# Kernel optimization log

Measured on AMD Instinct MI355X. Metric: run time of the kernel, lower is better.

## Reference

```python
import jax, jax.numpy as jnp
import numpy as np

NUM_USERS = 100000
NUM_ITEMS = 200000
IN_DIM = 128
HID = 256
E = 500000


def setup_inputs() -> dict:
    key = jax.random.key(0)
    ks = jax.random.split(key, 12)
    s1 = 1.0 / np.sqrt(2 * IN_DIM)
    s2 = 1.0 / np.sqrt(HID)
    return {
        "user_embed": jax.random.normal(ks[0], (NUM_USERS, IN_DIM), jnp.float32),
        "item_embed": jax.random.normal(ks[1], (NUM_ITEMS, IN_DIM), jnp.float32),
        "u_clicks": jax.random.randint(ks[2], (E,), 0, NUM_USERS, jnp.int32),
        "v_clicks": jax.random.randint(ks[3], (E,), 0, NUM_ITEMS, jnp.int32),
        "u_buys": jax.random.randint(ks[4], (E,), 0, NUM_USERS, jnp.int32),
        "v_buys": jax.random.randint(ks[5], (E,), 0, NUM_ITEMS, jnp.int32),
        "W1_clicks": jax.random.normal(ks[6], (2 * IN_DIM, HID), jnp.float32) * s1,
        "b1_clicks": jnp.zeros((HID,), jnp.float32),
        "W2_clicks": jax.random.normal(ks[7], (HID,), jnp.float32) * s2,
        "b2_clicks": jnp.zeros((1,), jnp.float32),
        "W1_buys": jax.random.normal(ks[8], (2 * IN_DIM, HID), jnp.float32) * s1,
        "b1_buys": jnp.zeros((HID,), jnp.float32),
        "W2_buys": jax.random.normal(ks[9], (HID,), jnp.float32) * s2,
        "b2_buys": jnp.zeros((1,), jnp.float32),
    }


def _edge_mlp(h_u, h_v, W1, b1, W2, b2):
    # concat([h_u, h_v]) @ W1 computed without materializing the concat:
    # split W1 into source-half and target-half. Dropout(p=0) is identity.
    d = h_u.shape[1]
    h = jax.nn.relu(h_u @ W1[:d] + h_v @ W1[d:] + b1)  # [E, HID]
    return h @ W2 + b2[0]  # [E] (Linear(hidden,1).squeeze(1))


def reference(user_embed, item_embed, u_clicks, v_clicks, u_buys, v_buys,
              W1_clicks, b1_clicks, W2_clicks, b2_clicks,
              W1_buys, b1_buys, W2_buys, b2_buys):
    logits_clicks = _edge_mlp(user_embed[u_clicks], item_embed[v_clicks],
                              W1_clicks, b1_clicks, W2_clicks, b2_clicks)
    logits_buys = _edge_mlp(user_embed[u_buys], item_embed[v_buys],
                            W1_buys, b1_buys, W2_buys, b2_buys)
    return logits_clicks, logits_buys
```

## Files before the change

### kernel.cpp

```cpp
#include <hip/hip_runtime.h>
#include <hip/hip_bf16.h>

typedef short bf16x8 __attribute__((ext_vector_type(8)));
typedef float f32x4 __attribute__((ext_vector_type(4)));

#define HID 256
#define IN_DIM 128
#define M_BLOCK 64

__device__ __forceinline__ float bf2f(unsigned short x) {
    union { unsigned int u; float f; } c; c.u = ((unsigned int)x) << 16; return c.f;
}
__device__ __forceinline__ unsigned short f2bf(float f) {
    union { float f; unsigned int u; } c; c.f = f;
    unsigned int u = c.u;
    u += 0x7FFFu + ((u >> 16) & 1u);
    return (unsigned short)(u >> 16);
}
__device__ __forceinline__ unsigned int pack2(float lo, float hi) {
    return (unsigned int)f2bf(lo) | ((unsigned int)f2bf(hi) << 16);
}

__device__ __forceinline__ void gload_lds16(const void* g, void* l) {
    __builtin_amdgcn_global_load_lds(
        (const __attribute__((address_space(1))) void*)g,
        (__attribute__((address_space(3))) void*)l,
        16, 0, 0);
}

__device__ __forceinline__ bool detect_bf16(const unsigned short* p, int strideElems) {
    const int lane = threadIdx.x & 63;
    unsigned int u = p[(size_t)2 * lane * strideElems];
    unsigned int e = (u >> 7) & 0xFFu;
    bool bad = ((u & 0x7FFFu) != 0u) && (e < 90u || e > 141u);
    return __ballot(bad) == 0ull;
}
__device__ __forceinline__ bool detect_idx64(const int* p) {
    const int lane = threadIdx.x & 63;
    int v = p[2 * (lane * 64) + 1];
    return __ballot(v != 0) == 0ull;
}

extern "C" __global__ void cvt_tables_kernel(
    const void* __restrict__ user_embed, const void* __restrict__ item_embed,
    unsigned short* __restrict__ uT, unsigned short* __restrict__ iT,
    long long nU8, long long nI8)
{
    const int t = blockIdx.y;
    const void* src = t ? item_embed : user_embed;
    unsigned short* dst = t ? iT : uT;
    const long long n8 = t ? nI8 : nU8;
    const bool bf = detect_bf16((const unsigned short*)src, 1024);
    long long i = (long long)blockIdx.x * 256 + threadIdx.x;
    const long long stride = (long long)gridDim.x * 256;
    if (bf) {
        const uint4* s = (const uint4*)src;
        for (; i < n8; i += stride)
            *reinterpret_cast<uint4*>(dst + i * 8) = s[i];
    } else {
        const float4* s = (const float4*)src;
        for (; i < n8; i += stride) {
            float4 f0 = s[2 * i];
            float4 f1 = s[2 * i + 1];
            uint4 o;
            o.x = pack2(f0.x, f0.y);
            o.y = pack2(f0.z, f0.w);
            o.z = pack2(f1.x, f1.y);
            o.w = pack2(f1.z, f1.w);
            *reinterpret_cast<uint4*>(dst + i * 8) = o;
        }
    }
}

extern "C" __global__ void pack_w1_kernel(
    const void* __restrict__ W1c,
    const void* __restrict__ W1b,
    unsigned short* __restrict__ outp)
{
    const int t = blockIdx.y;
    const void* W1 = t ? W1b : W1c;
    const unsigned short* W1u = (const unsigned short*)W1;
    const float* W1f = (const float*)W1;
    const bool w1bf = detect_bf16(W1u, 512);

    const int tid = blockIdx.x * 256 + threadIdx.x;
    const int lane = tid & 63;
    const int nt = (tid >> 6) & 15;
    const int kt = tid >> 10;
    const int k0 = kt * 32 + (lane >> 4) * 8;
    const int n  = nt * 16 + (lane & 15);
    unsigned short vals[8];
#pragma unroll
    for (int j = 0; j < 8; ++j) {
        const int src = (k0 + j) * HID + n;
        vals[j] = w1bf ? W1u[src] : f2bf(W1f[src]);
    }
    unsigned short* dst = outp + (size_t)t * 65536 + (size_t)tid * 8;
    *reinterpret_cast<uint4*>(dst) = *reinterpret_cast<const uint4*>(vals);
}

extern "C" __global__ __launch_bounds__(256, 4)
void edge_mlp_kernel(
    const void* __restrict__ user_embed,
    const void* __restrict__ item_embed,
    const unsigned short* __restrict__ uT,
    const unsigned short* __restrict__ iT,
    const int* __restrict__ u0, const int* __restrict__ v0,
    const int* __restrict__ u1, const int* __restrict__ v1,
    const unsigned short* __restrict__ packedW1,
    const void* __restrict__ b1_0, const void* __restrict__ w2_0,
    const void* __restrict__ b2_0,
    const void* __restrict__ b1_1, const void* __restrict__ w2_1,
    const void* __restrict__ b2_1,
    float* __restrict__ out, int E, int useWs)
{
    __shared__ __attribute__((aligned(16))) unsigned short sA[32 * 64 * 8];
    __shared__ float pRed[4][M_BLOCK];

    const int t  = blockIdx.y;
    const int e0 = blockIdx.x * M_BLOCK;
    const int tid = threadIdx.x;
    const int lane = tid & 63;
    const int wv = tid >> 6;

    const int* uI = t ? u1 : u0;
    const int* vI = t ? v1 : v0;
    const void* b1 = t ? b1_1 : b1_0;
    const void* w2 = t ? w2_1 : w2_0;
    const void* b2 = t ? b2_1 : b2_0;
    const unsigned short* pW = packedW1 + (size_t)t * 65536;

    const bool w2Bf = detect_bf16((const unsigned short*)w2, 2);

    {
        const int* gI = (wv < 2) ? uI : vI;
        const bool g64 = detect_idx64(gI);
        const int e = e0 + lane;
        const int eC = (e < E) ? e : (E - 1);
        const size_t idx = (size_t)(g64 ? gI[2 * eC] : gI[eC]);

        if (useWs) {
            const unsigned short* tab = (wv < 2) ? uT : iT;
            const unsigned short* rowbase = tab + idx * IN_DIM + (wv & 1) * 64;
            unsigned short* sbase = &sA[(wv * 8) * 512];
#pragma unroll
            for (int c = 0; c < 8; ++c)
                gload_lds16(rowbase + c * 8, sbase + c * 512);
        } else {
            const void* tab = (wv < 2) ? user_embed : item_embed;
            const bool tbf = detect_bf16((const unsigned short*)tab, 1024);
            if (tbf) {
                const unsigned short* rowbase =
                    (const unsigned short*)tab + idx * IN_DIM + (wv & 1) * 64;
                unsigned short* sbase = &sA[(wv * 8) * 512];
#pragma unroll
                for (int c = 0; c < 8; ++c)
                    gload_lds16(rowbase + c * 8, sbase + c * 512);
            } else {
                const float* rowbase =
                    (const float*)tab + idx * IN_DIM + (wv & 1) * 64;
#pragma unroll
                for (int c = 0; c < 8; ++c) {
                    float4 f0 = *reinterpret_cast<const float4*>(rowbase + c * 8);
                    float4 f1 = *reinterpret_cast<const float4*>(rowbase + c * 8 + 4);
                    uint4 o;
                    o.x = pack2(f0.x, f0.y);
                    o.y = pack2(f0.z, f0.w);
                    o.z = pack2(f1.x, f1.y);
                    o.w = pack2(f1.z, f1.w);
                    *reinterpret_cast<uint4*>(&sA[((wv * 8 + c) * 64 + lane) * 8]) = o;
                }
            }
        }
    }
    __syncthreads();

    const int lq = lane >> 4;
    const int lm = lane & 15;

    f32x4 acc[4][4];
#pragma unroll
    for (int ms = 0; ms < 4; ++ms)
#pragma unroll
        for (int ntg = 0; ntg < 4; ++ntg)
            acc[ms][ntg] = (f32x4){0.f, 0.f, 0.f, 0.f};

#pragma unroll
    for (int kt = 0; kt < 8; ++kt) {
        bf16x8 aF[4];
#pragma unroll
        for (int ms = 0; ms < 4; ++ms)
            aF[ms] = *reinterpret_cast<const bf16x8*>(
                &sA[(((kt * 4 + lq) * 64) + ms * 16 + lm) * 8]);
#pragma unroll
        for (int ntg = 0; ntg < 4; ++ntg) {
            const int nt = wv * 4 + ntg;
            bf16x8 bF = *reinterpret_cast<const bf16x8*>(
                pW + (((size_t)(kt * 16 + nt) * 64 + lane) * 8));
#pragma unroll
            for (int ms = 0; ms < 4; ++ms)
                acc[ms][ntg] = __builtin_amdgcn_mfma_f32_16x16x32_bf16(
                    aF[ms], bF, acc[ms][ntg], 0, 0, 0);
        }
    }

    float part[4][4];
#pragma unroll
    for (int ms = 0; ms < 4; ++ms)
#pragma unroll
        for (int r = 0; r < 4; ++r) part[ms][r] = 0.f;

#pragma unroll
    for (int ntg = 0; ntg < 4; ++ntg) {
        const int n = (wv * 4 + ntg) * 16 + lm;
        const float b1n = w2Bf ? bf2f(((const unsigned short*)b1)[n]) : ((const float*)b1)[n];
        const float w2n = w2Bf ? bf2f(((const unsigned short*)w2)[n]) : ((const float*)w2)[n];
#pragma unroll
        for (int ms = 0; ms < 4; ++ms)
#pragma unroll
            for (int r = 0; r < 4; ++r) {
                float h = acc[ms][ntg][r] + b1n;
                h = fmaxf(h, 0.f);
                part[ms][r] = fmaf(h, w2n, part[ms][r]);
            }
    }

#pragma unroll
    for (int off = 1; off < 16; off <<= 1) {
#pragma unroll
        for (int ms = 0; ms < 4; ++ms)
#pragma unroll
            for (int r = 0; r < 4; ++r)
                part[ms][r] += __shfl_xor(part[ms][r], off, 64);
    }

    if (lm == 0) {
#pragma unroll
        for (int ms = 0; ms < 4; ++ms)
#pragma unroll
            for (int r = 0; r < 4; ++r)
                pRed[wv][ms * 16 + lq * 4 + r] = part[ms][r];
    }
    __syncthreads();

    if (tid < M_BLOCK) {
        const int e = e0 + tid;
        if (e < E) {
            const float b2v = w2Bf ? bf2f(((const unsigned short*)b2)[0]) : ((const float*)b2)[0];
            float s = b2v + pRed[0][tid] + pRed[1][tid] + pRed[2][tid] + pRed[3][tid];
            out[(size_t)t * E + e] = s;
        }
    }
}

extern "C" void kernel_launch(void* const* d_in, const int* in_sizes, int n_in,
                              void* d_out, int out_size, void* d_ws, size_t ws_size,
                              hipStream_t stream)
{
    const void* user_embed = d_in[0];
    const void* item_embed = d_in[1];
    const int* u0 = (const int*)d_in[2];
    const int* v0 = (const int*)d_in[3];
    const int* u1 = (const int*)d_in[4];
    const int* v1 = (const int*)d_in[5];
    const void* W1c = d_in[6];
    const void* b1c = d_in[7];
    const void* w2c = d_in[8];
    const void* b2c = d_in[9];
    const void* W1b = d_in[10];
    const void* b1b = d_in[11];
    const void* w2b = d_in[12];
    const void* b2b = d_in[13];

    const int E = in_sizes[2];
    const size_t U = (size_t)in_sizes[0] / IN_DIM;
    const size_t I = (size_t)in_sizes[1] / IN_DIM;

    unsigned short* packedW1 = (unsigned short*)d_ws;
    unsigned short* uT = (unsigned short*)((char*)d_ws + 262144);
    unsigned short* iT = uT + U * IN_DIM;
    const size_t need = 262144 + (U + I) * IN_DIM * sizeof(unsigned short);
    const int useWs = (ws_size >= need) ? 1 : 0;

    if (useWs) {
        const long long nU8 = (long long)U * IN_DIM / 8;
        const long long nI8 = (long long)I * IN_DIM / 8;
        hipLaunchKernelGGL(cvt_tables_kernel, dim3(4096, 2), dim3(256), 0, stream,
                           user_embed, item_embed, uT, iT, nU8, nI8);
    }

    hipLaunchKernelGGL(pack_w1_kernel, dim3(32, 2), dim3(256), 0, stream, W1c, W1b, packedW1);

    dim3 grid((E + M_BLOCK - 1) / M_BLOCK, 2);
    hipLaunchKernelGGL(edge_mlp_kernel, grid, dim3(256), 0, stream,
                       user_embed, item_embed, uT, iT, u0, v0, u1, v1, packedW1,
                       b1c, w2c, b2c, b1b, w2b, b2b,
                       (float*)d_out, E, useWs);
}
```

Measured before the change: 424.8 us.

## Make edge MLP persistent with double-buffered gather and register-resident W1

```diff
diff --git a/kernel.cpp b/kernel.cpp
--- a/kernel.cpp
+++ b/kernel.cpp
@@ -3,10 +3,12 @@
 
 typedef short bf16x8 __attribute__((ext_vector_type(8)));
 typedef float f32x4 __attribute__((ext_vector_type(4)));
+typedef unsigned int u32x4 __attribute__((ext_vector_type(4)));
 
 #define HID 256
 #define IN_DIM 128
 #define M_BLOCK 64
+#define NPERSIST 256
 
 __device__ __forceinline__ float bf2f(unsigned short x) {
     union { unsigned int u; float f; } c; c.u = ((unsigned int)x) << 16; return c.f;
@@ -54,20 +56,20 @@
     long long i = (long long)blockIdx.x * 256 + threadIdx.x;
     const long long stride = (long long)gridDim.x * 256;
     if (bf) {
-        const uint4* s = (const uint4*)src;
+        const u32x4* s = (const u32x4*)src;
         for (; i < n8; i += stride)
-            *reinterpret_cast<uint4*>(dst + i * 8) = s[i];
+            __builtin_nontemporal_store(s[i], reinterpret_cast<u32x4*>(dst + i * 8));
     } else {
         const float4* s = (const float4*)src;
         for (; i < n8; i += stride) {
             float4 f0 = s[2 * i];
             float4 f1 = s[2 * i + 1];
-            uint4 o;
+            u32x4 o;
             o.x = pack2(f0.x, f0.y);
             o.y = pack2(f0.z, f0.w);
             o.z = pack2(f1.x, f1.y);
             o.w = pack2(f1.z, f1.w);
-            *reinterpret_cast<uint4*>(dst + i * 8) = o;
+            __builtin_nontemporal_store(o, reinterpret_cast<u32x4*>(dst + i * 8));
         }
     }
 }
@@ -99,7 +101,7 @@
     *reinterpret_cast<uint4*>(dst) = *reinterpret_cast<const uint4*>(vals);
 }
 
-extern "C" __global__ __launch_bounds__(256, 4)
+extern "C" __global__ __launch_bounds__(256, 2)
 void edge_mlp_kernel(
     const void* __restrict__ user_embed,
     const void* __restrict__ item_embed,
@@ -114,14 +116,15 @@
     const void* __restrict__ b2_1,
     float* __restrict__ out, int E, int useWs)
 {
-    __shared__ __attribute__((aligned(16))) unsigned short sA[32 * 64 * 8];
+    __shared__ __attribute__((aligned(16))) unsigned short sA[2][32 * 64 * 8];
     __shared__ float pRed[4][M_BLOCK];
 
-    const int t  = blockIdx.y;
-    const int e0 = blockIdx.x * M_BLOCK;
+    const int t   = blockIdx.y;
     const int tid = threadIdx.x;
     const int lane = tid & 63;
-    const int wv = tid >> 6;
+    const int wv   = tid >> 6;
+    const int lq = lane >> 4;
+    const int lm = lane & 15;
 
     const int* uI = t ? u1 : u0;
     const int* vI = t ? v1 : v0;
@@ -132,124 +135,143 @@
 
     const bool w2Bf = detect_bf16((const unsigned short*)w2, 2);
 
-    {
-        const int* gI = (wv < 2) ? uI : vI;
-        const bool g64 = detect_idx64(gI);
-        const int e = e0 + lane;
+    const int* gI = (wv < 2) ? uI : vI;
+    const bool g64 = detect_idx64(gI);
+    const int halfOff = (wv & 1) * 64;
+    const unsigned short* tabW = (wv < 2) ? uT : iT;
+    const void* tabRaw = (wv < 2) ? user_embed : item_embed;
+    bool tbf = false;
+    if (!useWs) tbf = detect_bf16((const unsigned short*)tabRaw, 1024);
+
+    bf16x8 bFr[8][4];
+#pragma unroll
+    for (int kt = 0; kt < 8; ++kt)
+#pragma unroll
+        for (int ntg = 0; ntg < 4; ++ntg)
+            bFr[kt][ntg] = *reinterpret_cast<const bf16x8*>(
+                pW + (((size_t)(kt * 16 + wv * 4 + ntg) * 64 + lane) * 8));
+
+    float b1v[4], w2v[4];
+#pragma unroll
+    for (int ntg = 0; ntg < 4; ++ntg) {
+        const int n = (wv * 4 + ntg) * 16 + lm;
+        b1v[ntg] = w2Bf ? bf2f(((const unsigned short*)b1)[n]) : ((const float*)b1)[n];
+        w2v[ntg] = w2Bf ? bf2f(((const unsigned short*)w2)[n]) : ((const float*)w2)[n];
+    }
+    const float b2v = w2Bf ? bf2f(((const unsigned short*)b2)[0]) : ((const float*)b2)[0];
+
+    const int ntiles = (E + M_BLOCK - 1) / M_BLOCK;
+
+    auto gather_tile = [&](int tile, int buf) {
+        const int e = tile * M_BLOCK + lane;
         const int eC = (e < E) ? e : (E - 1);
         const size_t idx = (size_t)(g64 ? gI[2 * eC] : gI[eC]);
-
+        unsigned short* sbase = &sA[buf][(wv * 8) * 512];
         if (useWs) {
-            const unsigned short* tab = (wv < 2) ? uT : iT;
-            const unsigned short* rowbase = tab + idx * IN_DIM + (wv & 1) * 64;
-            unsigned short* sbase = &sA[(wv * 8) * 512];
+            const unsigned short* rowbase = tabW + idx * IN_DIM + halfOff;
+#pragma unroll
+            for (int c = 0; c < 8; ++c)
+                gload_lds16(rowbase + c * 8, sbase + c * 512);
+        } else if (tbf) {
+            const unsigned short* rowbase =
+                (const unsigned short*)tabRaw + idx * IN_DIM + halfOff;
 #pragma unroll
             for (int c = 0; c < 8; ++c)
                 gload_lds16(rowbase + c * 8, sbase + c * 512);
         } else {
-            const void* tab = (wv < 2) ? user_embed : item_embed;
-            const bool tbf = detect_bf16((const unsigned short*)tab, 1024);
-            if (tbf) {
-                const unsigned short* rowbase =
-                    (const unsigned short*)tab + idx * IN_DIM + (wv & 1) * 64;
-                unsigned short* sbase = &sA[(wv * 8) * 512];
-#pragma unroll
-                for (int c = 0; c < 8; ++c)
-                    gload_lds16(rowbase + c * 8, sbase + c * 512);
-            } else {
-                const float* rowbase =
-                    (const float*)tab + idx * IN_DIM + (wv & 1) * 64;
-#pragma unroll
-                for (int c = 0; c < 8; ++c) {
-                    float4 f0 = *reinterpret_cast<const float4*>(rowbase + c * 8);
-                    float4 f1 = *reinterpret_cast<const float4*>(rowbase + c * 8 + 4);
-                    uint4 o;
-                    o.x = pack2(f0.x, f0.y);
-                    o.y = pack2(f0.z, f0.w);
-                    o.z = pack2(f1.x, f1.y);
-                    o.w = pack2(f1.z, f1.w);
-                    *reinterpret_cast<uint4*>(&sA[((wv * 8 + c) * 64 + lane) * 8]) = o;
+            const float* rowbase = (const float*)tabRaw + idx * IN_DIM + halfOff;
+#pragma unroll
+            for (int c = 0; c < 8; ++c) {
+                float4 f0 = *reinterpret_cast<const float4*>(rowbase + c * 8);
+                float4 f1 = *reinterpret_cast<const float4*>(rowbase + c * 8 + 4);
+                uint4 o;
+                o.x = pack2(f0.x, f0.y);
+                o.y = pack2(f0.z, f0.w);
+                o.z = pack2(f1.x, f1.y);
+                o.w = pack2(f1.z, f1.w);
+                *reinterpret_cast<uint4*>(sbase + c * 512 + lane * 8) = o;
+            }
+        }
+    };
+
+    int ti = blockIdx.x;
+    int cur = 0;
+    if (ti < ntiles) gather_tile(ti, 0);
+    __syncthreads();
+
+    while (ti < ntiles) {
+        const int tn = ti + gridDim.x;
+        if (tn < ntiles) gather_tile(tn, cur ^ 1);
+
+        f32x4 acc[4][4];
+#pragma unroll
+        for (int ms = 0; ms < 4; ++ms)
+#pragma unroll
+            for (int ntg = 0; ntg < 4; ++ntg)
+                acc[ms][ntg] = (f32x4){0.f, 0.f, 0.f, 0.f};
+
+        const unsigned short* sAc = sA[cur];
+#pragma unroll
+        for (int kt = 0; kt < 8; ++kt) {
+            bf16x8 aF[4];
+#pragma unroll
+            for (int ms = 0; ms < 4; ++ms)
+                aF[ms] = *reinterpret_cast<const bf16x8*>(
+                    &sAc[(((kt * 4 + lq) * 64) + ms * 16 + lm) * 8]);
+#pragma unroll
+            for (int ntg = 0; ntg < 4; ++ntg)
+#pragma unroll
+                for (int ms = 0; ms < 4; ++ms)
+                    acc[ms][ntg] = __builtin_amdgcn_mfma_f32_16x16x32_bf16(
+                        aF[ms], bFr[kt][ntg], acc[ms][ntg], 0, 0, 0);
+        }
+
+        float part[4][4];
+#pragma unroll
+        for (int ms = 0; ms < 4; ++ms)
+#pragma unroll
+            for (int r = 0; r < 4; ++r) part[ms][r] = 0.f;
+
+#pragma unroll
+        for (int ntg = 0; ntg < 4; ++ntg)
+#pragma unroll
+            for (int ms = 0; ms < 4; ++ms)
+#pragma unroll
+                for (int r = 0; r < 4; ++r) {
+                    float h = acc[ms][ntg][r] + b1v[ntg];
+                    h = fmaxf(h, 0.f);
+                    part[ms][r] = fmaf(h, w2v[ntg], part[ms][r]);
                 }
+
+#pragma unroll
+        for (int off = 1; off < 16; off <<= 1) {
+#pragma unroll
+            for (int ms = 0; ms < 4; ++ms)
+#pragma unroll
+                for (int r = 0; r < 4; ++r)
+                    part[ms][r] += __shfl_xor(part[ms][r], off, 64);
+        }
+
+        if (lm == 0) {
+#pragma unroll
+            for (int ms = 0; ms < 4; ++ms)
+#pragma unroll
+                for (int r = 0; r < 4; ++r)
+                    pRed[wv][ms * 16 + lq * 4 + r] = part[ms][r];
+        }
+        __syncthreads();
+
+        if (tid < M_BLOCK) {
+            const int e = ti * M_BLOCK + tid;
+            if (e < E) {
+                float s = b2v + pRed[0][tid] + pRed[1][tid] + pRed[2][tid] + pRed[3][tid];
+                out[(size_t)t * E + e] = s;
             }
         }
-    }
-    __syncthreads();
-
-    const int lq = lane >> 4;
-    const int lm = lane & 15;
-
-    f32x4 acc[4][4];
-#pragma unroll
-    for (int ms = 0; ms < 4; ++ms)
-#pragma unroll
-        for (int ntg = 0; ntg < 4; ++ntg)
-            acc[ms][ntg] = (f32x4){0.f, 0.f, 0.f, 0.f};
-
-#pragma unroll
-    for (int kt = 0; kt < 8; ++kt) {
-        bf16x8 aF[4];
-#pragma unroll
-        for (int ms = 0; ms < 4; ++ms)
-            aF[ms] = *reinterpret_cast<const bf16x8*>(
-                &sA[(((kt * 4 + lq) * 64) + ms * 16 + lm) * 8]);
-#pragma unroll
-        for (int ntg = 0; ntg < 4; ++ntg) {
-            const int nt = wv * 4 + ntg;
-            bf16x8 bF = *reinterpret_cast<const bf16x8*>(
-                pW + (((size_t)(kt * 16 + nt) * 64 + lane) * 8));
-#pragma unroll
-            for (int ms = 0; ms < 4; ++ms)
-                acc[ms][ntg] = __builtin_amdgcn_mfma_f32_16x16x32_bf16(
-                    aF[ms], bF, acc[ms][ntg], 0, 0, 0);
-        }
-    }
-
-    float part[4][4];
-#pragma unroll
-    for (int ms = 0; ms < 4; ++ms)
-#pragma unroll
-        for (int r = 0; r < 4; ++r) part[ms][r] = 0.f;
-
-#pragma unroll
-    for (int ntg = 0; ntg < 4; ++ntg) {
-        const int n = (wv * 4 + ntg) * 16 + lm;
-        const float b1n = w2Bf ? bf2f(((const unsigned short*)b1)[n]) : ((const float*)b1)[n];
-        const float w2n = w2Bf ? bf2f(((const unsigned short*)w2)[n]) : ((const float*)w2)[n];
-#pragma unroll
-        for (int ms = 0; ms < 4; ++ms)
-#pragma unroll
-            for (int r = 0; r < 4; ++r) {
-                float h = acc[ms][ntg][r] + b1n;
-                h = fmaxf(h, 0.f);
-                part[ms][r] = fmaf(h, w2n, part[ms][r]);
-            }
-    }
-
-#pragma unroll
-    for (int off = 1; off < 16; off <<= 1) {
-#pragma unroll
-        for (int ms = 0; ms < 4; ++ms)
-#pragma unroll
-            for (int r = 0; r < 4; ++r)
-                part[ms][r] += __shfl_xor(part[ms][r], off, 64);
-    }
-
-    if (lm == 0) {
-#pragma unroll
-        for (int ms = 0; ms < 4; ++ms)
-#pragma unroll
-            for (int r = 0; r < 4; ++r)
-                pRed[wv][ms * 16 + lq * 4 + r] = part[ms][r];
-    }
-    __syncthreads();
-
-    if (tid < M_BLOCK) {
-        const int e = e0 + tid;
-        if (e < E) {
-            const float b2v = w2Bf ? bf2f(((const unsigned short*)b2)[0]) : ((const float*)b2)[0];
-            float s = b2v + pRed[0][tid] + pRed[1][tid] + pRed[2][tid] + pRed[3][tid];
-            out[(size_t)t * E + e] = s;
-        }
+        __syncthreads();
+
+        ti = tn;
+        cur ^= 1;
     }
 }
 
@@ -285,14 +307,13 @@
     if (useWs) {
         const long long nU8 = (long long)U * IN_DIM / 8;
         const long long nI8 = (long long)I * IN_DIM / 8;
-        hipLaunchKernelGGL(cvt_tables_kernel, dim3(4096, 2), dim3(256), 0, stream,
+        hipLaunchKernelGGL(cvt_tables_kernel, dim3(2048, 2), dim3(256), 0, stream,
                            user_embed, item_embed, uT, iT, nU8, nI8);
     }
 
     hipLaunchKernelGGL(pack_w1_kernel, dim3(32, 2), dim3(256), 0, stream, W1c, W1b, packedW1);
 
-    dim3 grid((E + M_BLOCK - 1) / M_BLOCK, 2);
-    hipLaunchKernelGGL(edge_mlp_kernel, grid, dim3(256), 0, stream,
+    hipLaunchKernelGGL(edge_mlp_kernel, dim3(NPERSIST, 2), dim3(256), 0, stream,
                        user_embed, item_embed, uT, iT, u0, v0, u1, v1, packedW1,
                        b1c, w2c, b2c, b1b, w2b, b2b,
                        (float*)d_out, E, useWs);
```

Result: no change. 430.7 us (+1.4%).
